# Performance work log

Measured on AMD Instinct MI355X. Metric: run time of the kernel, lower is better.

The kernel has to match this reference:

```python
import jax, jax.numpy as jnp
import numpy as np

B, T, C = 2, 1024, 2048
HEAD = 64              # args.head_size_a
H = C // HEAD          # n_head = 32
D_DECAY, D_AAA, D_MV, D_GATE = 96, 96, 64, 256
GN_EPS = 0.00064
EPS_NORM = 1e-12

ARGS = ['x', 'v0', 'xx_r', 'xx_w', 'xx_k', 'xx_v', 'xx_a', 'xx_g',
        'ww_b', 'ww_w1', 'ww_w2', 'aa_b', 'aa_w1', 'aa_w2',
        'vv_b', 'vv_w1', 'vv_w2', 'gg_w1', 'gg_w2',
        'kk_s', 'ka_s', 'rk_s', 'W_r', 'W_k', 'W_v', 'W_o', 'gn_w', 'gn_b']


def setup_inputs() -> dict:
    key = jax.random.key(0)
    it = iter(jax.random.split(key, 32))
    nrm = lambda shape, s=1.0: jax.random.normal(next(it), shape, jnp.float32) * s
    d = {'x': nrm((B, T, C)), 'v0': nrm((B, T, C))}
    for nm in ('xx_r', 'xx_w', 'xx_k', 'xx_v', 'xx_a', 'xx_g',
               'ww_b', 'aa_b', 'vv_b', 'kk_s', 'ka_s'):
        d[nm] = nrm((1, 1, C), 0.5)
    d['ww_w1'] = nrm((C, D_DECAY), 0.02); d['ww_w2'] = nrm((D_DECAY, C), 0.02)
    d['aa_w1'] = nrm((C, D_AAA), 0.02);   d['aa_w2'] = nrm((D_AAA, C), 0.02)
    d['vv_w1'] = nrm((C, D_MV), 0.02);    d['vv_w2'] = nrm((D_MV, C), 0.02)
    d['gg_w1'] = nrm((C, D_GATE), 0.02);  d['gg_w2'] = nrm((D_GATE, C), 0.02)
    d['rk_s'] = nrm((H, HEAD), 0.5)
    d['W_r'] = nrm((C, C), 0.02); d['W_k'] = nrm((C, C), 0.02)
    d['W_v'] = nrm((C, C), 0.02); d['W_o'] = nrm((C, C), 0.02)
    d['gn_w'] = jnp.ones((C,), jnp.float32)
    d['gn_b'] = jnp.zeros((C,), jnp.float32)
    return d


def _rwkv7_op(r, w, k, v, a, b):
    # RWKV7 state recurrence: state[b,h,i,j] (i = value dim, j = key dim),
    # vectorized over (B,H,N), scanned over T.
    to_tbhn = lambda t: t.reshape(B, T, H, HEAD).astype(jnp.float32).transpose(1, 0, 2, 3)
    rT, kT, vT, aT, bT = map(to_tbhn, (r, k, v, a, b))
    wT = jnp.exp(-jnp.exp(to_tbhn(w)))   # decay in (0, 1)
    state0 = jnp.zeros((B, H, HEAD, HEAD), jnp.float32)

    def step(state, inp):
        wt, kt, vt, at, bt, rt = inp     # each [B,H,N]
        sa = jnp.einsum('bhij,bhj->bhi', state, at)
        state = (state * wt[:, :, None, :]
                 + sa[..., None] * bt[:, :, None, :]
                 + vt[..., None] * kt[:, :, None, :])
        return state, jnp.einsum('bhij,bhj->bhi', state, rt)

    _, outs = jax.lax.scan(step, state0, (wT, kT, vT, aT, bT, rT))  # [T,B,H,N]
    return outs.transpose(1, 0, 2, 3).reshape(B, T, C)


def _group_norm(y, gn_w, gn_b):
    # GroupNorm(H, C, eps=0.00064) applied on (B*T, C): per-(token, head) stats over N
    yh = y.reshape(B, T, H, HEAD)
    mu = yh.mean(-1, keepdims=True)
    var = yh.var(-1, keepdims=True)
    yh = (yh - mu) * jax.lax.rsqrt(var + GN_EPS)
    yh = yh * gn_w.reshape(1, 1, H, HEAD) + gn_b.reshape(1, 1, H, HEAD)
    return yh.reshape(B, T, C)


def _forward(x, v0, xx_r, xx_w, xx_k, xx_v, xx_a, xx_g,
             ww_b, ww_w1, ww_w2, aa_b, aa_w1, aa_w2,
             vv_b, vv_w1, vv_w2, gg_w1, gg_w2,
             kk_s, ka_s, rk_s, W_r, W_k, W_v, W_o, gn_w, gn_b):
    # time_shift(x) - x : shift sequence right by one with zero pad
    xx = jnp.pad(x, ((0, 0), (1, 0), (0, 0)))[:, :T, :] - x
    xr = x + xx * xx_r; xw = x + xx * xx_w; xk = x + xx * xx_k
    xv = x + xx * xx_v; xa = x + xx * xx_a; xg = x + xx * xx_g

    r = xr @ W_r
    w = -jax.nn.softplus(-(ww_b + jnp.tanh(xw @ ww_w1) @ ww_w2)) - 0.5  # clamp to (-inf,-0.5)
    k = xk @ W_k
    v = xv @ W_v
    # layer_id > 0: mix with layer-0 value residual
    v = v + (v0 - v) * jax.nn.sigmoid(vv_b + (xv @ vv_w1) @ vv_w2)
    a = jax.nn.sigmoid(aa_b + (xa @ aa_w1) @ aa_w2)
    g = jax.nn.sigmoid(xg @ gg_w1) @ gg_w2

    kk = k * kk_s
    kkh = kk.reshape(B, T, H, HEAD)
    kk = (kkh / jnp.maximum(jnp.linalg.norm(kkh, axis=-1, keepdims=True), EPS_NORM)).reshape(B, T, C)
    k = k * (1.0 + (a - 1.0) * ka_s)

    y = _rwkv7_op(r, w, k, v, -kk, kk * a)
    y = _group_norm(y, gn_w, gn_b)
    # per-head bonus: (r*k*rk_s).sum(-1) * v
    bonus = ((r.reshape(B, T, H, HEAD) * k.reshape(B, T, H, HEAD) * rk_s).sum(-1, keepdims=True)
             * v.reshape(B, T, H, HEAD)).reshape(B, T, C)
    y = y + bonus
    return (y * g) @ W_o


def reference(x, v0, xx_r, xx_w, xx_k, xx_v, xx_a, xx_g,
              ww_b, ww_w1, ww_w2, aa_b, aa_w1, aa_w2,
              vv_b, vv_w1, vv_w2, gg_w1, gg_w2,
              kk_s, ka_s, rk_s, W_r, W_k, W_v, W_o, gn_w, gn_b):
    out = _forward(x, v0, xx_r, xx_w, xx_k, xx_v, xx_a, xx_g,
                   ww_b, ww_w1, ww_w2, aa_b, aa_w1, aa_w2,
                   vv_b, vv_w1, vv_w2, gg_w1, gg_w2,
                   kk_s, ka_s, rk_s, W_r, W_k, W_v, W_o, gn_w, gn_b)
    # layer_id > 0 passes v0 through unchanged
    return (out, v0)
```

## Files before the change

kernel.cpp:

```cpp
#include <hip/hip_runtime.h>
#include <hip/hip_bf16.h>
#include <math.h>

typedef unsigned short u16;
typedef __attribute__((ext_vector_type(4))) unsigned short us4;
typedef __attribute__((ext_vector_type(8))) unsigned short us8;
typedef __attribute__((ext_vector_type(8))) short s8v;
typedef __attribute__((ext_vector_type(4))) float f4v;

#define BB 2
#define TT 1024
#define CC 2048
#define HH 32
#define BT (BB*TT)


__device__ __forceinline__ float bf2f(u16 u) {
  return __uint_as_float(((unsigned int)u) << 16);
}
__device__ __forceinline__ u16 f2bf(float f) {
  unsigned int x = __float_as_uint(f);
  x += 0x7fffu + ((x >> 16) & 1u);
  return (u16)(x >> 16);
}

__global__ __launch_bounds__(256)
void mix_k(const float* __restrict__ x, const float* __restrict__ s,
           u16* __restrict__ out) {
  int idx = blockIdx.x * 256 + threadIdx.x;
  int c = idx & (CC - 1);
  int t = (idx >> 11) & (TT - 1);
  float xv = x[idx];
  float xp = (t == 0) ? 0.f : x[idx - CC];
  out[idx] = f2bf(xv + (xp - xv) * s[c]);
}

__global__ __launch_bounds__(256)
void wt_k(const float* __restrict__ W, u16* __restrict__ Wt, int K, int N) {
  __shared__ u16 tile[32][36];
  const int k0 = blockIdx.x * 32, n0 = blockIdx.y * 32;
  const int tid = threadIdx.x;
  const int r = tid >> 3, c4 = (tid & 7) << 2;
  float4 v = *(const float4*)(W + (size_t)(k0 + r) * N + n0 + c4);
  tile[r][c4 + 0] = f2bf(v.x); tile[r][c4 + 1] = f2bf(v.y);
  tile[r][c4 + 2] = f2bf(v.z); tile[r][c4 + 3] = f2bf(v.w);
  __syncthreads();
  ushort4 o;
  o.x = tile[c4 + 0][r]; o.y = tile[c4 + 1][r];
  o.z = tile[c4 + 2][r]; o.w = tile[c4 + 3][r];
  *(ushort4*)(Wt + (size_t)(n0 + r) * K + k0 + c4) = o;
}

enum { EPI_BF = 0, EPI_F32 = 1, EPI_BIAS_SP = 2, EPI_BIAS_SIG = 3,
       EPI_VMIX = 4 };

template<int EPI>
__global__ __launch_bounds__(256)
void mgemm_k(const u16* __restrict__ A, const u16* __restrict__ Bt,
             float* __restrict__ outF, u16* __restrict__ outB,
             int M, int N, int K,
             const float* __restrict__ bias, const u16* __restrict__ p1,
             const float* __restrict__ p2)
{
  __shared__ alignas(16) u16 As[128][40];
  __shared__ alignas(16) u16 Bs[128][40];
  const int m0 = blockIdx.x * 128;
  const int n0 = blockIdx.y * 128;
  const int tid = threadIdx.x;
  const int lane = tid & 63;
  const int wid = tid >> 6;
  const int wr = wid >> 1, wc = wid & 1;
  const int srow = tid >> 1;
  const int scol = (tid & 1) << 4;
  f4v acc[4][4];
  #pragma unroll
  for (int i = 0; i < 4; ++i)
    #pragma unroll
    for (int j = 0; j < 4; ++j) acc[i][j] = f4v{0.f, 0.f, 0.f, 0.f};

  const int l15 = lane & 15;
  const int lk = (lane >> 4) << 3;
  const int nkt = K >> 5;
  for (int kt = 0; kt < nkt; ++kt) {
    const int k0 = kt << 5;
    const u16* ap = A  + (size_t)(m0 + srow) * K + k0 + scol;
    const u16* bp = Bt + (size_t)(n0 + srow) * K + k0 + scol;
    us8 a0 = *(const us8*)(ap);
    us8 a1 = *(const us8*)(ap + 8);
    us8 b0 = *(const us8*)(bp);
    us8 b1 = *(const us8*)(bp + 8);
    __syncthreads();
    *(us8*)&As[srow][scol]     = a0;
    *(us8*)&As[srow][scol + 8] = a1;
    *(us8*)&Bs[srow][scol]     = b0;
    *(us8*)&Bs[srow][scol + 8] = b1;
    __syncthreads();
    s8v af[4], bfr[4];
    #pragma unroll
    for (int i = 0; i < 4; ++i)
      af[i] = *(const s8v*)&As[wr * 64 + i * 16 + l15][lk];
    #pragma unroll
    for (int j = 0; j < 4; ++j)
      bfr[j] = *(const s8v*)&Bs[wc * 64 + j * 16 + l15][lk];
    #pragma unroll
    for (int i = 0; i < 4; ++i)
      #pragma unroll
      for (int j = 0; j < 4; ++j)
        acc[i][j] = __builtin_amdgcn_mfma_f32_16x16x32_bf16(af[i], bfr[j],
                                                            acc[i][j], 0, 0, 0);
  }
  const int rbase = m0 + wr * 64 + ((lane >> 4) << 2);
  const int cbase = n0 + wc * 64 + l15;
  #pragma unroll
  for (int i = 0; i < 4; ++i) {
    #pragma unroll
    for (int j = 0; j < 4; ++j) {
      f4v c = acc[i][j];
      const int col = cbase + j * 16;
      #pragma unroll
      for (int q = 0; q < 4; ++q) {
        const int row = rbase + i * 16 + q;
        const size_t idx = (size_t)row * N + col;
        const float r = c[q];
        if (EPI == EPI_BF) {
          outB[idx] = f2bf(r);
        } else if (EPI == EPI_F32) {
          outF[idx] = r;
        } else if (EPI == EPI_BIAS_SP) {
          float u = bias[col] + r;
          float z = -u;
          float sp = fmaxf(z, 0.f) + log1pf(expf(-fabsf(z)));
          outB[idx] = f2bf(-sp - 0.5f);
        } else if (EPI == EPI_BIAS_SIG) {
          float u = bias[col] + r;
          outB[idx] = f2bf(1.f / (1.f + expf(-u)));
        } else if (EPI == EPI_VMIX) {
          float u = bias[col] + r;
          float sg = 1.f / (1.f + expf(-u));
          float v = bf2f(p1[idx]);
          float v0v = p2[idx];
          outB[idx] = f2bf(v + (v0v - v) * sg);
        }
      }
    }
  }
}

__global__ __launch_bounds__(256)
void gemm_part_k(const u16* __restrict__ A, const float* __restrict__ W,
                 float* __restrict__ outF, int M, int N, int K, int kchunk,
                 int NP)
{
  __shared__ alignas(16) float As[16][68];
  __shared__ alignas(16) float Bs[16][68];
  const int m0 = blockIdx.x * 64;
  const int n0 = blockIdx.y * 64;
  const int kz = blockIdx.z;
  const int k0base = kz * kchunk;
  const int tid = threadIdx.x;
  const int tx = tid & 15, ty = tid >> 4;
  float acc[4][4] = {{0.f}};
  const int a_m = tid >> 2;
  const int a_k = (tid & 3) << 2;
  const int b_k = tid >> 4;
  const int b_n = (tid & 15) << 2;
  const int niters = kchunk >> 4;
  for (int it = 0; it < niters; ++it) {
    const int k0 = k0base + (it << 4);
    float4 av;
    {
      ushort4 u = *(const ushort4*)(A + (size_t)(m0 + a_m) * K + (k0 + a_k));
      av = make_float4(bf2f(u.x), bf2f(u.y), bf2f(u.z), bf2f(u.w));
    }
    float4 bv;
    {
      int gn = n0 + b_n;
      const float* wp = W + (size_t)(k0 + b_k) * N + gn;
      if (gn + 3 < N) {
        bv = *(const float4*)wp;
      } else {
        bv.x = (gn + 0 < N) ? wp[0] : 0.f;
        bv.y = (gn + 1 < N) ? wp[1] : 0.f;
        bv.z = (gn + 2 < N) ? wp[2] : 0.f;
        bv.w = (gn + 3 < N) ? wp[3] : 0.f;
      }
    }
    __syncthreads();
    As[a_k + 0][a_m] = av.x; As[a_k + 1][a_m] = av.y;
    As[a_k + 2][a_m] = av.z; As[a_k + 3][a_m] = av.w;
    Bs[b_k][b_n + 0] = bv.x; Bs[b_k][b_n + 1] = bv.y;
    Bs[b_k][b_n + 2] = bv.z; Bs[b_k][b_n + 3] = bv.w;
    __syncthreads();
    #pragma unroll
    for (int kk = 0; kk < 16; ++kk) {
      float4 a4 = *(const float4*)&As[kk][ty << 2];
      float4 b4 = *(const float4*)&Bs[kk][tx << 2];
      float ar[4] = {a4.x, a4.y, a4.z, a4.w};
      float br[4] = {b4.x, b4.y, b4.z, b4.w};
      #pragma unroll
      for (int i = 0; i < 4; ++i)
        #pragma unroll
        for (int j = 0; j < 4; ++j)
          acc[i][j] = fmaf(ar[i], br[j], acc[i][j]);
    }
  }
  #pragma unroll
  for (int i = 0; i < 4; ++i) {
    int gm = m0 + (ty << 2) + i;
    #pragma unroll
    for (int j = 0; j < 4; ++j) {
      int gn = n0 + (tx << 2) + j;
      if (gn >= N) continue;
      outF[((size_t)kz * M + gm) * NP + gn] = acc[i][j];
    }
  }
}

__global__ __launch_bounds__(256)
void reduce_k(const float* __restrict__ part, u16* __restrict__ out,
              int M, int D, int NP, int nz, int act)
{
  int idx = blockIdx.x * 256 + threadIdx.x;
  if (idx >= M * D) return;
  int t = idx / D, n = idx - t * D;
  float s = 0.f;
  for (int z = 0; z < nz; ++z) s += part[((size_t)z * M + t) * NP + n];
  if (act == 1) s = tanhf(s);
  else if (act == 2) s = 1.f / (1.f + expf(-s));
  out[idx] = f2bf(s);
}

__global__ __launch_bounds__(256)
void prep_k(const u16* __restrict__ k_in, const u16* __restrict__ a_in,
            const u16* __restrict__ r_in, const u16* __restrict__ w_in,
            const float* __restrict__ kk_s, const float* __restrict__ ka_s,
            u16* __restrict__ ao_out, u16* __restrict__ bo_out,
            u16* __restrict__ k_out, u16* __restrict__ wd_out,
            u16* __restrict__ rw_out, float* __restrict__ scal)
{
  int tid = threadIdx.x;
  int lane = tid & 63;
  int wv = tid >> 6;
  int hidx = blockIdx.x * 4 + wv;
  int h = hidx & (HH - 1);
  int c = (h << 6) + lane;
  size_t base = ((size_t)hidx << 6) + lane;
  float k = bf2f(k_in[base]);
  float kk = k * kk_s[c];
  float ss = kk * kk;
  for (int off = 32; off; off >>= 1) ss += __shfl_xor(ss, off, 64);
  float kkn = kk / fmaxf(sqrtf(ss), 1e-12f);
  float a = bf2f(a_in[base]);
  float r = bf2f(r_in[base]);
  float kf = k * (1.f + (a - 1.f) * ka_s[c]);
  float wd = expf(-expf(bf2f(w_in[base])));
  float bo = kkn * a;
  ao_out[base] = f2bf(-kkn);
  bo_out[base] = f2bf(bo);
  k_out[base]  = f2bf(kf);
  wd_out[base] = f2bf(wd);
  rw_out[base] = f2bf(wd * r);
  float kr = kf * r, br = bo * r;
  kr += __shfl_xor(kr, 1, 64);  br += __shfl_xor(br, 1, 64);
  kr += __shfl_xor(kr, 2, 64);  br += __shfl_xor(br, 2, 64);
  kr += __shfl_xor(kr, 4, 64);  br += __shfl_xor(br, 4, 64);
  kr += __shfl_xor(kr, 8, 64);  br += __shfl_xor(br, 8, 64);
  kr += __shfl_xor(kr, 16, 64); br += __shfl_xor(br, 16, 64);
  kr += __shfl_xor(kr, 32, 64); br += __shfl_xor(br, 32, 64);
  if (lane == 0) {
    scal[hidx] = kr;
    scal[(size_t)BT * HH + hidx] = br;
  }
}

__global__ __launch_bounds__(256)
void rec_k(const u16* __restrict__ rw, const u16* __restrict__ wd,
           const u16* __restrict__ kv, const u16* __restrict__ v,
           const u16* __restrict__ ao, const u16* __restrict__ bo,
           const float* __restrict__ scal, u16* __restrict__ y)
{
  const int gw = blockIdx.x * 4 + (threadIdx.x >> 6);
  const int lane = threadIdx.x & 63;
  const int sub = lane & 15;
  const int grp = lane >> 4;
  const int bh = gw >> 4;
  const int rblk = gw & 15;
  const int i = rblk * 4 + grp;
  const int b = bh >> 5, h = bh & (HH - 1);
  const size_t base0 = ((size_t)b * TT) * CC + (h << 6);
  const size_t vecb = base0 + (sub << 2);
  const size_t vb   = base0 + i;
  const int sbase = b * TT * HH + h;
  float s0 = 0.f, s1 = 0.f, s2 = 0.f, s3 = 0.f;
  us4 pwd = *(const us4*)(wd + vecb);
  us4 pk  = *(const us4*)(kv + vecb);
  us4 pao = *(const us4*)(ao + vecb);
  us4 pbo = *(const us4*)(bo + vecb);
  us4 prw = *(const us4*)(rw + vecb);
  float pv  = bf2f(v[vb]);
  float pkr = scal[sbase];
  float pbr = scal[(size_t)BT * HH + sbase];
  for (int t = 0; t < TT; ++t) {
    const float w0 = bf2f(pwd[0]), w1 = bf2f(pwd[1]),
                w2 = bf2f(pwd[2]), w3 = bf2f(pwd[3]);
    const float q0 = bf2f(pk[0]),  q1 = bf2f(pk[1]),
                q2 = bf2f(pk[2]),  q3 = bf2f(pk[3]);
    const float a0 = bf2f(pao[0]), a1 = bf2f(pao[1]),
                a2 = bf2f(pao[2]), a3 = bf2f(pao[3]);
    const float c0 = bf2f(pbo[0]), c1 = bf2f(pbo[1]),
                c2 = bf2f(pbo[2]), c3 = bf2f(pbo[3]);
    const float e0 = bf2f(prw[0]), e1 = bf2f(prw[1]),
                e2 = bf2f(prw[2]), e3 = bf2f(prw[3]);
    const float cv = pv, ckr = pkr, cbr = pbr;
    if (t + 1 < TT) {
      const size_t nb = vecb + (size_t)(t + 1) * CC;
      pwd = *(const us4*)(wd + nb);
      pk  = *(const us4*)(kv + nb);
      pao = *(const us4*)(ao + nb);
      pbo = *(const us4*)(bo + nb);
      prw = *(const us4*)(rw + nb);
      pv  = bf2f(v[vb + (size_t)(t + 1) * CC]);
      pkr = scal[sbase + (t + 1) * HH];
      pbr = scal[(size_t)BT * HH + sbase + (t + 1) * HH];
    }
    float sa = fmaf(s3, a3, fmaf(s2, a2, fmaf(s1, a1, s0 * a0)));
    float yw = fmaf(s3, e3, fmaf(s2, e2, fmaf(s1, e1, s0 * e0)));
    sa += __shfl_xor(sa, 1, 64);  yw += __shfl_xor(yw, 1, 64);
    sa += __shfl_xor(sa, 2, 64);  yw += __shfl_xor(yw, 2, 64);
    sa += __shfl_xor(sa, 4, 64);  yw += __shfl_xor(yw, 4, 64);
    sa += __shfl_xor(sa, 8, 64);  yw += __shfl_xor(yw, 8, 64);
    s0 = fmaf(cv, q0, fmaf(sa, c0, s0 * w0));
    s1 = fmaf(cv, q1, fmaf(sa, c1, s1 * w1));
    s2 = fmaf(cv, q2, fmaf(sa, c2, s2 * w2));
    s3 = fmaf(cv, q3, fmaf(sa, c3, s3 * w3));
    float o = fmaf(cv, ckr, fmaf(sa, cbr, yw));
    if (sub == 0) y[vb + (size_t)t * CC] = f2bf(o);
  }
}

__global__ __launch_bounds__(256)
void gn_k(u16* __restrict__ y, const u16* __restrict__ r,
          const u16* __restrict__ k, const u16* __restrict__ v,
          const u16* __restrict__ g, const float* __restrict__ rk_s,
          const float* __restrict__ gn_w, const float* __restrict__ gn_b)
{
  int tid = threadIdx.x, lane = tid & 63, wv = tid >> 6;
  int hidx = blockIdx.x * 4 + wv;
  int h = hidx & (HH - 1);
  int c = (h << 6) + lane;
  size_t base = ((size_t)hidx << 6) + lane;
  float yv = bf2f(y[base]), rv = bf2f(r[base]), kv = bf2f(k[base]);
  float vv = bf2f(v[base]), gv = bf2f(g[base]);
  float bsum = rv * kv * rk_s[c];
  float s1 = yv, s2 = yv * yv;
  for (int off = 32; off; off >>= 1) {
    s1 += __shfl_xor(s1, off, 64);
    s2 += __shfl_xor(s2, off, 64);
    bsum += __shfl_xor(bsum, off, 64);
  }
  float mu = s1 * (1.f / 64.f);
  float var = s2 * (1.f / 64.f) - mu * mu;
  float rstd = rsqrtf(var + 0.00064f);
  float z = (yv - mu) * rstd * gn_w[c] + gn_b[c];
  y[base] = f2bf((z + bsum * vv) * gv);
}

__global__ __launch_bounds__(256)
void copy_v0(const float* __restrict__ v0, float* __restrict__ out) {
  int idx = blockIdx.x * 256 + threadIdx.x;
  ((float4*)out)[idx] = ((const float4*)v0)[idx];
}

__global__ __launch_bounds__(256)
void zero_out(float* __restrict__ out) {
  int idx = blockIdx.x * 256 + threadIdx.x;
  ((float4*)out)[idx] = make_float4(0.f, 0.f, 0.f, 0.f);
}

extern "C" void kernel_launch(void* const* d_in, const int* in_sizes, int n_in,
                              void* d_out, int out_size, void* d_ws, size_t ws_size,
                              hipStream_t stream) {
  (void)n_in; (void)out_size;
  const bool dictOrder = (in_sizes[9] == CC);
  int IX[28];
  if (dictOrder) {
    const int m[28] = {0,1,2,3,4,5,6,7, 8,13,14, 9,15,16, 10,17,18, 19,20,
                       11,12,21, 22,23,24,25, 26,27};
    for (int i = 0; i < 28; ++i) IX[i] = m[i];
  } else {
    for (int i = 0; i < 28; ++i) IX[i] = i;
  }
  const float* x     = (const float*)d_in[IX[0]];
  const float* v0    = (const float*)d_in[IX[1]];
  const float* xx_r  = (const float*)d_in[IX[2]];
  const float* xx_w  = (const float*)d_in[IX[3]];
  const float* xx_k  = (const float*)d_in[IX[4]];
  const float* xx_v  = (const float*)d_in[IX[5]];
  const float* xx_a  = (const float*)d_in[IX[6]];
  const float* xx_g  = (const float*)d_in[IX[7]];
  const float* ww_b  = (const float*)d_in[IX[8]];
  const float* ww_w1 = (const float*)d_in[IX[9]];
  const float* ww_w2 = (const float*)d_in[IX[10]];
  const float* aa_b  = (const float*)d_in[IX[11]];
  const float* aa_w1 = (const float*)d_in[IX[12]];
  const float* aa_w2 = (const float*)d_in[IX[13]];
  const float* vv_b  = (const float*)d_in[IX[14]];
  const float* vv_w1 = (const float*)d_in[IX[15]];
  const float* vv_w2 = (const float*)d_in[IX[16]];
  const float* gg_w1 = (const float*)d_in[IX[17]];
  const float* gg_w2 = (const float*)d_in[IX[18]];
  const float* kk_s  = (const float*)d_in[IX[19]];
  const float* ka_s  = (const float*)d_in[IX[20]];
  const float* rk_s  = (const float*)d_in[IX[21]];
  const float* W_r   = (const float*)d_in[IX[22]];
  const float* W_k   = (const float*)d_in[IX[23]];
  const float* W_v   = (const float*)d_in[IX[24]];
  const float* W_o   = (const float*)d_in[IX[25]];
  const float* gn_w  = (const float*)d_in[IX[26]];
  const float* gn_b  = (const float*)d_in[IX[27]];

  const size_t NBTC = (size_t)BT * CC;
  dim3 blk(256);
  const int grid4f = (int)(NBTC / 4 / 256);

  const size_t WS_NEED = 7 * NBTC * sizeof(u16);
  float* outF = (float*)d_out;
  if (ws_size < WS_NEED || d_ws == nullptr) {
    zero_out<<<grid4f, blk, 0, stream>>>(outF);
    copy_v0<<<grid4f, blk, 0, stream>>>(v0, outF + NBTC);
    return;
  }

  u16* W16   = (u16*)d_ws;
  u16* R0 = W16 + 0 * NBTC;
  u16* R1 = W16 + 1 * NBTC;
  u16* R2 = W16 + 2 * NBTC;
  u16* R3 = W16 + 3 * NBTC;
  u16* R4 = W16 + 4 * NBTC;
  u16* R5 = W16 + 5 * NBTC;
  u16* R6 = W16 + 6 * NBTC;
  float* partY = (float*)R3;
  float* partG = (float*)R5;
  u16* ws_y = (u16*)(outF + NBTC);
  float* scal = (float*)(ws_y + NBTC);

  const int gridMix = (BT * CC) / 256;
  dim3 gM(BT / 128, 2048 / 128);

  mix_k<<<gridMix, blk, 0, stream>>>(x, xx_w, R6);
  gemm_part_k<<<dim3(32, 2, 8), blk, 0, stream>>>(R6, ww_w1, partY,
      BT, 96, 2048, 256, 128);
  reduce_k<<<(BT * 96 + 255) / 256, blk, 0, stream>>>(partY, R0, BT, 96, 128, 8, 1);
  wt_k<<<dim3(3, 64), blk, 0, stream>>>(ww_w2, R1, 96, 2048);
  mgemm_k<EPI_BIAS_SP><<<gM, blk, 0, stream>>>(R0, R1, nullptr, R5,
      BT, 2048, 96, ww_b, nullptr, nullptr);

  mix_k<<<gridMix, blk, 0, stream>>>(x, xx_a, R6);
  gemm_part_k<<<dim3(32, 2, 8), blk, 0, stream>>>(R6, aa_w1, partY,
      BT, 96, 2048, 256, 128);
  reduce_k<<<(BT * 96 + 255) / 256, blk, 0, stream>>>(partY, R0, BT, 96, 128, 8, 0);
  wt_k<<<dim3(3, 64), blk, 0, stream>>>(aa_w2, R1, 96, 2048);
  mgemm_k<EPI_BIAS_SIG><<<gM, blk, 0, stream>>>(R0, R1, nullptr, R4,
      BT, 2048, 96, aa_b, nullptr, nullptr);

  mix_k<<<gridMix, blk, 0, stream>>>(x, xx_v, R6);
  wt_k<<<dim3(64, 64), blk, 0, stream>>>(W_v, R1, 2048, 2048);
  mgemm_k<EPI_BF><<<gM, blk, 0, stream>>>(R6, R1, nullptr, R2,
      BT, 2048, 2048, nullptr, nullptr, nullptr);
  gemm_part_k<<<dim3(32, 1, 8), blk, 0, stream>>>(R6, vv_w1, partY,
      BT, 64, 2048, 256, 64);
  reduce_k<<<(BT * 64 + 255) / 256, blk, 0, stream>>>(partY, R0, BT, 64, 64, 8, 0);
  wt_k<<<dim3(2, 64), blk, 0, stream>>>(vv_w2, R1, 64, 2048);
  mgemm_k<EPI_VMIX><<<gM, blk, 0, stream>>>(R0, R1, nullptr, R2,
      BT, 2048, 64, vv_b, R2, v0);

  mix_k<<<gridMix, blk, 0, stream>>>(x, xx_k, R6);
  wt_k<<<dim3(64, 64), blk, 0, stream>>>(W_k, R3, 2048, 2048);
  mgemm_k<EPI_BF><<<gM, blk, 0, stream>>>(R6, R3, nullptr, R1,
      BT, 2048, 2048, nullptr, nullptr, nullptr);

  mix_k<<<gridMix, blk, 0, stream>>>(x, xx_r, R6);
  wt_k<<<dim3(64, 64), blk, 0, stream>>>(W_r, R3, 2048, 2048);
  mgemm_k<EPI_BF><<<gM, blk, 0, stream>>>(R6, R3, nullptr, R0,
      BT, 2048, 2048, nullptr, nullptr, nullptr);

  prep_k<<<BT * HH / 4, blk, 0, stream>>>(R1, R4, R0, R5, kk_s, ka_s,
                                          R3, R4, R1, R5, R6, scal);

  rec_k<<<256, blk, 0, stream>>>(R6, R5, R1, R2, R3, R4, scal, ws_y);

  mix_k<<<gridMix, blk, 0, stream>>>(x, xx_g, R6);
  gemm_part_k<<<dim3(32, 4, 2), blk, 0, stream>>>(R6, gg_w1, partG,
      BT, 256, 2048, 1024, 256);
  reduce_k<<<(BT * 256 + 255) / 256, blk, 0, stream>>>(partG, R3, BT, 256, 256, 2, 2);
  wt_k<<<dim3(8, 64), blk, 0, stream>>>(gg_w2, R5, 256, 2048);
  mgemm_k<EPI_BF><<<gM, blk, 0, stream>>>(R3, R5, nullptr, R4,
      BT, 2048, 256, nullptr, nullptr, nullptr);

  gn_k<<<BT * HH / 4, blk, 0, stream>>>(ws_y, R0, R1, R2, R4,
                                        rk_s, gn_w, gn_b);

  wt_k<<<dim3(64, 64), blk, 0, stream>>>(W_o, R5, 2048, 2048);
  mgemm_k<EPI_F32><<<gM, blk, 0, stream>>>(ws_y, R5, outF, nullptr,
      BT, 2048, 2048, nullptr, nullptr, nullptr);

  copy_v0<<<grid4f, blk, 0, stream>>>(v0, outF + NBTC);
}
```

Baseline: 980.5 us.

## Fuse two recurrence timesteps per iteration via precomputed pairwise coefficients

```diff
diff --git a/kernel.cpp b/kernel.cpp
--- a/kernel.cpp
+++ b/kernel.cpp
@@ -236,7 +236,7 @@
             const float* __restrict__ kk_s, const float* __restrict__ ka_s,
             u16* __restrict__ ao_out, u16* __restrict__ bo_out,
             u16* __restrict__ k_out, u16* __restrict__ wd_out,
-            u16* __restrict__ rw_out, float* __restrict__ scal)
+            u16* __restrict__ rw_out, float2* __restrict__ scal)
 {
   int tid = threadIdx.x;
   int lane = tid & 63;
@@ -267,17 +267,49 @@
   kr += __shfl_xor(kr, 8, 64);  br += __shfl_xor(br, 8, 64);
   kr += __shfl_xor(kr, 16, 64); br += __shfl_xor(br, 16, 64);
   kr += __shfl_xor(kr, 32, 64); br += __shfl_xor(br, 32, 64);
-  if (lane == 0) {
-    scal[hidx] = kr;
-    scal[(size_t)BT * HH + hidx] = br;
-  }
+  if (lane == 0) scal[hidx] = make_float2(kr, br);
+}
+
+__global__ __launch_bounds__(256)
+void prep2_k(u16* __restrict__ wd, u16* __restrict__ ao,
+             u16* __restrict__ bo, u16* __restrict__ rw,
+             const u16* __restrict__ kf, float4* __restrict__ scal4)
+{
+  int tid = threadIdx.x;
+  int lane = tid & 63;
+  int wv = tid >> 6;
+  int hpidx = blockIdx.x * 4 + wv;
+  int h = hpidx & (HH - 1);
+  int btp = hpidx >> 5;
+  int tp = btp & (TT / 2 - 1);
+  int b = btp >> 9;
+  size_t be = ((size_t)(b * TT + 2 * tp)) * CC + (h << 6) + lane;
+  size_t bodd = be + CC;
+  float wd1 = bf2f(wd[be]),  wd2 = bf2f(wd[bodd]);
+  float ao2 = bf2f(ao[bodd]), rw2 = bf2f(rw[bodd]);
+  float bo1 = bf2f(bo[be]),  k1  = bf2f(kf[be]);
+  float cba = bo1 * ao2, ckb = k1 * ao2, crb = bo1 * rw2, crk = k1 * rw2;
+  #pragma unroll
+  for (int off = 32; off; off >>= 1) {
+    cba += __shfl_xor(cba, off, 64);
+    ckb += __shfl_xor(ckb, off, 64);
+    crb += __shfl_xor(crb, off, 64);
+    crk += __shfl_xor(crk, off, 64);
+  }
+  wd[be]   = f2bf(wd1 * wd2);
+  wd[bodd] = f2bf(k1 * wd2);
+  ao[bodd] = f2bf(wd1 * ao2);
+  bo[be]   = f2bf(bo1 * wd2);
+  rw[bodd] = f2bf(wd1 * rw2);
+  if (lane == 0) scal4[hpidx] = make_float4(cba, ckb, crb, crk);
 }
 
 __global__ __launch_bounds__(256)
 void rec_k(const u16* __restrict__ rw, const u16* __restrict__ wd,
            const u16* __restrict__ kv, const u16* __restrict__ v,
            const u16* __restrict__ ao, const u16* __restrict__ bo,
-           const float* __restrict__ scal, u16* __restrict__ y)
+           const float2* __restrict__ scal, const float4* __restrict__ scal4,
+           u16* __restrict__ y)
 {
   const int gw = blockIdx.x * 4 + (threadIdx.x >> 6);
   const int lane = threadIdx.x & 63;
@@ -291,51 +323,76 @@
   const size_t vecb = base0 + (sub << 2);
   const size_t vb   = base0 + i;
   const int sbase = b * TT * HH + h;
+  const int pbase = b * (TT / 2) * HH + h;
   float s0 = 0.f, s1 = 0.f, s2 = 0.f, s3 = 0.f;
-  us4 pwd = *(const us4*)(wd + vecb);
-  us4 pk  = *(const us4*)(kv + vecb);
-  us4 pao = *(const us4*)(ao + vecb);
-  us4 pbo = *(const us4*)(bo + vecb);
-  us4 prw = *(const us4*)(rw + vecb);
-  float pv  = bf2f(v[vb]);
-  float pkr = scal[sbase];
-  float pbr = scal[(size_t)BT * HH + sbase];
-  for (int t = 0; t < TT; ++t) {
-    const float w0 = bf2f(pwd[0]), w1 = bf2f(pwd[1]),
-                w2 = bf2f(pwd[2]), w3 = bf2f(pwd[3]);
-    const float q0 = bf2f(pk[0]),  q1 = bf2f(pk[1]),
-                q2 = bf2f(pk[2]),  q3 = bf2f(pk[3]);
-    const float a0 = bf2f(pao[0]), a1 = bf2f(pao[1]),
-                a2 = bf2f(pao[2]), a3 = bf2f(pao[3]);
-    const float c0 = bf2f(pbo[0]), c1 = bf2f(pbo[1]),
-                c2 = bf2f(pbo[2]), c3 = bf2f(pbo[3]);
-    const float e0 = bf2f(prw[0]), e1 = bf2f(prw[1]),
-                e2 = bf2f(prw[2]), e3 = bf2f(prw[3]);
-    const float cv = pv, ckr = pkr, cbr = pbr;
-    if (t + 1 < TT) {
-      const size_t nb = vecb + (size_t)(t + 1) * CC;
-      pwd = *(const us4*)(wd + nb);
-      pk  = *(const us4*)(kv + nb);
-      pao = *(const us4*)(ao + nb);
-      pbo = *(const us4*)(bo + nb);
-      prw = *(const us4*)(rw + nb);
-      pv  = bf2f(v[vb + (size_t)(t + 1) * CC]);
-      pkr = scal[sbase + (t + 1) * HH];
-      pbr = scal[(size_t)BT * HH + sbase + (t + 1) * HH];
+
+  us4 W12, KW1, AO1, WA2, BW1, BO2, RW1, WR2, K2;
+  float V1, V2; float2 SE, SO; float4 S4;
+#define PLOAD(TP) do {                                                  \
+    const size_t be_ = vecb + (size_t)(2 * (TP)) * CC;                  \
+    const size_t bo_ = be_ + CC;                                        \
+    W12 = *(const us4*)(wd + be_);  KW1 = *(const us4*)(wd + bo_);      \
+    AO1 = *(const us4*)(ao + be_);  WA2 = *(const us4*)(ao + bo_);      \
+    BW1 = *(const us4*)(bo + be_);  BO2 = *(const us4*)(bo + bo_);      \
+    RW1 = *(const us4*)(rw + be_);  WR2 = *(const us4*)(rw + bo_);      \
+    K2  = *(const us4*)(kv + bo_);                                      \
+    V1 = bf2f(v[vb + (size_t)(2 * (TP)) * CC]);                         \
+    V2 = bf2f(v[vb + (size_t)(2 * (TP) + 1) * CC]);                     \
+    SE = scal[sbase + (2 * (TP)) * HH];                                 \
+    SO = scal[sbase + (2 * (TP) + 1) * HH];                             \
+    S4 = scal4[pbase + (TP) * HH];                                      \
+  } while (0)
+
+  PLOAD(0);
+  for (int tp = 0; tp < TT / 2; ++tp) {
+    const float w0 = bf2f(W12[0]), w1 = bf2f(W12[1]),
+                w2 = bf2f(W12[2]), w3 = bf2f(W12[3]);
+    const float kw0 = bf2f(KW1[0]), kw1_ = bf2f(KW1[1]),
+                kw2 = bf2f(KW1[2]), kw3 = bf2f(KW1[3]);
+    const float a0 = bf2f(AO1[0]), a1 = bf2f(AO1[1]),
+                a2 = bf2f(AO1[2]), a3 = bf2f(AO1[3]);
+    const float x0 = bf2f(WA2[0]), x1 = bf2f(WA2[1]),
+                x2 = bf2f(WA2[2]), x3 = bf2f(WA2[3]);
+    const float bw0 = bf2f(BW1[0]), bw1_ = bf2f(BW1[1]),
+                bw2 = bf2f(BW1[2]), bw3 = bf2f(BW1[3]);
+    const float b0 = bf2f(BO2[0]), b1 = bf2f(BO2[1]),
+                b2 = bf2f(BO2[2]), b3 = bf2f(BO2[3]);
+    const float e0 = bf2f(RW1[0]), e1 = bf2f(RW1[1]),
+                e2 = bf2f(RW1[2]), e3 = bf2f(RW1[3]);
+    const float f0 = bf2f(WR2[0]), f1 = bf2f(WR2[1]),
+                f2 = bf2f(WR2[2]), f3 = bf2f(WR2[3]);
+    const float k0 = bf2f(K2[0]), k1 = bf2f(K2[1]),
+                k2 = bf2f(K2[2]), k3 = bf2f(K2[3]);
+    const float v1c = V1, v2c = V2;
+    const float kr1 = SE.x, br1 = SE.y, kr2 = SO.x, br2 = SO.y;
+    const float cba = S4.x, ckb = S4.y, crb = S4.z, crk = S4.w;
+    if (tp + 1 < TT / 2) PLOAD(tp + 1);
+    float u1 = fmaf(s3, a3, fmaf(s2, a2, fmaf(s1, a1, s0 * a0)));
+    float u2 = fmaf(s3, x3, fmaf(s2, x2, fmaf(s1, x1, s0 * x0)));
+    float q1 = fmaf(s3, e3, fmaf(s2, e2, fmaf(s1, e1, s0 * e0)));
+    float q2 = fmaf(s3, f3, fmaf(s2, f2, fmaf(s1, f1, s0 * f0)));
+    u1 += __shfl_xor(u1, 1, 64);  u2 += __shfl_xor(u2, 1, 64);
+    q1 += __shfl_xor(q1, 1, 64);  q2 += __shfl_xor(q2, 1, 64);
+    u1 += __shfl_xor(u1, 2, 64);  u2 += __shfl_xor(u2, 2, 64);
+    q1 += __shfl_xor(q1, 2, 64);  q2 += __shfl_xor(q2, 2, 64);
+    u1 += __shfl_xor(u1, 4, 64);  u2 += __shfl_xor(u2, 4, 64);
+    q1 += __shfl_xor(q1, 4, 64);  q2 += __shfl_xor(q2, 4, 64);
+    u1 += __shfl_xor(u1, 8, 64);  u2 += __shfl_xor(u2, 8, 64);
+    q1 += __shfl_xor(q1, 8, 64);  q2 += __shfl_xor(q2, 8, 64);
+    const float sac = fmaf(ckb, v1c, fmaf(cba, u1, u2));
+    const float y1 = fmaf(br1, u1, fmaf(kr1, v1c, q1));
+    const float y2 = fmaf(br2, sac, fmaf(kr2, v2c,
+                       fmaf(crb, u1, fmaf(crk, v1c, q2))));
+    s0 = fmaf(v2c, k0, fmaf(v1c, kw0, fmaf(sac, b0, fmaf(u1, bw0, s0 * w0))));
+    s1 = fmaf(v2c, k1, fmaf(v1c, kw1_, fmaf(sac, b1, fmaf(u1, bw1_, s1 * w1))));
+    s2 = fmaf(v2c, k2, fmaf(v1c, kw2, fmaf(sac, b2, fmaf(u1, bw2, s2 * w2))));
+    s3 = fmaf(v2c, k3, fmaf(v1c, kw3, fmaf(sac, b3, fmaf(u1, bw3, s3 * w3))));
+    if (sub == 0) {
+      y[vb + (size_t)(2 * tp) * CC] = f2bf(y1);
+      y[vb + (size_t)(2 * tp + 1) * CC] = f2bf(y2);
     }
-    float sa = fmaf(s3, a3, fmaf(s2, a2, fmaf(s1, a1, s0 * a0)));
-    float yw = fmaf(s3, e3, fmaf(s2, e2, fmaf(s1, e1, s0 * e0)));
-    sa += __shfl_xor(sa, 1, 64);  yw += __shfl_xor(yw, 1, 64);
-    sa += __shfl_xor(sa, 2, 64);  yw += __shfl_xor(yw, 2, 64);
-    sa += __shfl_xor(sa, 4, 64);  yw += __shfl_xor(yw, 4, 64);
-    sa += __shfl_xor(sa, 8, 64);  yw += __shfl_xor(yw, 8, 64);
-    s0 = fmaf(cv, q0, fmaf(sa, c0, s0 * w0));
-    s1 = fmaf(cv, q1, fmaf(sa, c1, s1 * w1));
-    s2 = fmaf(cv, q2, fmaf(sa, c2, s2 * w2));
-    s3 = fmaf(cv, q3, fmaf(sa, c3, s3 * w3));
-    float o = fmaf(cv, ckr, fmaf(sa, cbr, yw));
-    if (sub == 0) y[vb + (size_t)t * CC] = f2bf(o);
-  }
+  }
+#undef PLOAD
 }
 
 __global__ __launch_bounds__(256)
@@ -442,7 +499,8 @@
   float* partY = (float*)R3;
   float* partG = (float*)R5;
   u16* ws_y = (u16*)(outF + NBTC);
-  float* scal = (float*)(ws_y + NBTC);
+  float2* scal = (float2*)(ws_y + NBTC);
+  float4* scal4 = (float4*)(ws_y + NBTC + (size_t)BT * HH * 4);
 
   const int gridMix = (BT * CC) / 256;
   dim3 gM(BT / 128, 2048 / 128);
@@ -487,7 +545,9 @@
   prep_k<<<BT * HH / 4, blk, 0, stream>>>(R1, R4, R0, R5, kk_s, ka_s,
                                           R3, R4, R1, R5, R6, scal);
 
-  rec_k<<<256, blk, 0, stream>>>(R6, R5, R1, R2, R3, R4, scal, ws_y);
+  prep2_k<<<BT / 2 * HH / 4, blk, 0, stream>>>(R5, R3, R4, R6, R1, scal4);
+
+  rec_k<<<256, blk, 0, stream>>>(R6, R5, R1, R2, R3, R4, scal, scal4, ws_y);
 
   mix_k<<<gridMix, blk, 0, stream>>>(x, xx_g, R6);
   gemm_part_k<<<dim3(32, 4, 2), blk, 0, stream>>>(R6, gg_w1, partG,
```

After: 866.3 us. 11.6% less time.
